# Kernel tuning notes

Measured on AMD Instinct MI355X. Metric: run time of the kernel, lower is better.

Reference implementation:

```python
import jax, jax.numpy as jnp
import numpy as np

EPSILON = 0.1
MAX_ITERATIONS = 100


def setup_inputs() -> dict:
    key = jax.random.key(0)
    k1, k2 = jax.random.split(key)
    x = jax.random.normal(k1, (16, 3, 2048), dtype=jnp.float32)
    y = jax.random.normal(k2, (16, 3, 2048), dtype=jnp.float32)
    return {"x": x, "y": y}


def reference(x, y):
    # x, y: (B, D, N) channels-first point clouds -> (B, N, D)
    xt = jnp.swapaxes(x, 1, 2)
    yt = jnp.swapaxes(y, 1, 2)
    B, N, _ = xt.shape
    # squared euclidean cost: (B, N, N)
    x2 = jnp.sum(xt * xt, axis=-1)  # (B, N)
    y2 = jnp.sum(yt * yt, axis=-1)  # (B, N)
    C = x2[:, :, None] + y2[:, None, :] - 2.0 * jnp.einsum('bnd,bmd->bnm', xt, yt)
    C = jnp.maximum(C, 0.0)  # cdist clamps negatives from cancellation
    K = jnp.exp(-C / EPSILON)

    inv_n = 1.0 / N
    u0 = jnp.full((B, N), inv_n, dtype=x.dtype)
    v0 = jnp.full((B, N), inv_n, dtype=x.dtype)

    def step(carry, _):
        u, _v = carry
        v = inv_n / (jnp.einsum('bnm,bn->bm', K, u) + 1e-8)  # K^T u
        u = inv_n / (jnp.einsum('bnm,bm->bn', K, v) + 1e-8)  # K v
        return (u, v), None

    (u, v), _ = jax.lax.scan(step, (u0, v0), None, length=MAX_ITERATIONS)
    # sum(plan * C) / B where plan = u[:,:,None] * K * v[:,None,:]
    return jnp.einsum('bn,bnm,bm->', u, K * C, v) / B
```

## Files before the change

kernel.cpp:

```cpp
#include <hip/hip_runtime.h>
#include <hip/hip_bf16.h>

#define NB 16
#define NN 2048
#define G  64
#define ITERS 100

static constexpr float INV_N = 1.0f / (float)NN;
static constexpr float NEG_INV_EPS = -10.0f;

__device__ __forceinline__ float bfl(unsigned int p) { return __uint_as_float(p << 16); }
__device__ __forceinline__ float bfh(unsigned int p) { return __uint_as_float(p & 0xffff0000u); }
__device__ __forceinline__ unsigned short f2bf(float f) {
    unsigned int u = __float_as_uint(f);
    unsigned int r = (u + 0x7fffu + ((u >> 16) & 1u)) >> 16;
    return (unsigned short)r;
}
__device__ __forceinline__ float fastrcp(float x) { return __builtin_amdgcn_rcpf(x); }

__global__ __launch_bounds__(256) void build_K(const float* __restrict__ x,
                                               const float* __restrict__ y,
                                               unsigned short* __restrict__ K) {
    const int n = blockIdx.x, b = blockIdx.y, tid = threadIdx.x;
    const float* xb = x + (size_t)b * 3 * NN;
    const float* yb = y + (size_t)b * 3 * NN;
    const float x0 = xb[n], x1 = xb[NN + n], x2 = xb[2 * NN + n];
    const float xs = x0 * x0 + x1 * x1 + x2 * x2;
    const int m0 = tid * 8;

    const float4 a0 = *(const float4*)(yb + m0);
    const float4 a1 = *(const float4*)(yb + m0 + 4);
    const float4 b0 = *(const float4*)(yb + NN + m0);
    const float4 b1 = *(const float4*)(yb + NN + m0 + 4);
    const float4 c0 = *(const float4*)(yb + 2 * NN + m0);
    const float4 c1 = *(const float4*)(yb + 2 * NN + m0 + 4);
    const float yy0[8] = {a0.x, a0.y, a0.z, a0.w, a1.x, a1.y, a1.z, a1.w};
    const float yy1[8] = {b0.x, b0.y, b0.z, b0.w, b1.x, b1.y, b1.z, b1.w};
    const float yy2[8] = {c0.x, c0.y, c0.z, c0.w, c1.x, c1.y, c1.z, c1.w};

    unsigned short kk[8];
#pragma unroll
    for (int j = 0; j < 8; ++j) {
        const float ys  = yy0[j] * yy0[j] + yy1[j] * yy1[j] + yy2[j] * yy2[j];
        const float dot = x0 * yy0[j] + x1 * yy1[j] + x2 * yy2[j];
        const float C   = fmaxf(xs + ys - 2.0f * dot, 0.0f);
        kk[j] = f2bf(__expf(NEG_INV_EPS * C));
    }
    uint4 pk;
    pk.x = (unsigned int)kk[0] | ((unsigned int)kk[1] << 16);
    pk.y = (unsigned int)kk[2] | ((unsigned int)kk[3] << 16);
    pk.z = (unsigned int)kk[4] | ((unsigned int)kk[5] << 16);
    pk.w = (unsigned int)kk[6] | ((unsigned int)kk[7] << 16);
    *(uint4*)(K + ((size_t)(b * NN + n)) * NN + m0) = pk;
}

__global__ __launch_bounds__(256) void reduce_v(const float* __restrict__ PART,
                                                float* __restrict__ VV) {
    const int t = blockIdx.x * 256 + threadIdx.x;
    const int b = t >> 11, m = t & (NN - 1);
    const float* p = PART + (size_t)(b * G) * NN + m;
    float s = 0.0f;
#pragma unroll 8
    for (int g = 0; g < G; ++g) s += p[(size_t)g * NN];
    VV[t] = INV_N * fastrcp(s + 1e-8f);
}

__global__ __launch_bounds__(256) void fused_pass(const unsigned short* __restrict__ K,
                                                  const float* __restrict__ VV,
                                                  float* __restrict__ u_out,
                                                  float* __restrict__ PART,
                                                  int first) {
    const int g = blockIdx.x, b = blockIdx.y, tid = threadIdx.x;
    const int w = tid >> 6, l = tid & 63;

    float v[4][8];
    if (!first) {
        const float* vb = VV + b * NN;
#pragma unroll
        for (int s = 0; s < 4; ++s) {
            const float4 p0 = *(const float4*)(vb + s * 512 + l * 8);
            const float4 p1 = *(const float4*)(vb + s * 512 + l * 8 + 4);
            v[s][0] = p0.x; v[s][1] = p0.y; v[s][2] = p0.z; v[s][3] = p0.w;
            v[s][4] = p1.x; v[s][5] = p1.y; v[s][6] = p1.z; v[s][7] = p1.w;
        }
    }

    float acc[4][8];
#pragma unroll
    for (int s = 0; s < 4; ++s)
#pragma unroll
        for (int j = 0; j < 8; ++j) acc[s][j] = 0.0f;

#pragma unroll 2
    for (int r = 0; r < 8; ++r) {
        const int n = g * 32 + w * 8 + r;
        const unsigned short* Kp = K + ((size_t)(b * NN + n)) * NN + l * 8;
        uint4 kv[4];
#pragma unroll
        for (int s = 0; s < 4; ++s) kv[s] = *(const uint4*)(Kp + s * 512);

        float u;
        if (first) {
            u = INV_N;
        } else {
            float a0 = 0, a1 = 0, a2 = 0, a3 = 0, a4 = 0, a5 = 0, a6 = 0, a7 = 0;
#pragma unroll
            for (int s = 0; s < 4; ++s) {
                a0 = fmaf(bfl(kv[s].x), v[s][0], a0);
                a1 = fmaf(bfh(kv[s].x), v[s][1], a1);
                a2 = fmaf(bfl(kv[s].y), v[s][2], a2);
                a3 = fmaf(bfh(kv[s].y), v[s][3], a3);
                a4 = fmaf(bfl(kv[s].z), v[s][4], a4);
                a5 = fmaf(bfh(kv[s].z), v[s][5], a5);
                a6 = fmaf(bfl(kv[s].w), v[s][6], a6);
                a7 = fmaf(bfh(kv[s].w), v[s][7], a7);
            }
            float d = ((a0 + a1) + (a2 + a3)) + ((a4 + a5) + (a6 + a7));
#pragma unroll
            for (int off = 32; off > 0; off >>= 1) d += __shfl_xor(d, off, 64);
            u = INV_N * fastrcp(d + 1e-8f);
        }
        if (l == 0) u_out[b * NN + n] = u;

#pragma unroll
        for (int s = 0; s < 4; ++s) {
            acc[s][0] = fmaf(bfl(kv[s].x), u, acc[s][0]);
            acc[s][1] = fmaf(bfh(kv[s].x), u, acc[s][1]);
            acc[s][2] = fmaf(bfl(kv[s].y), u, acc[s][2]);
            acc[s][3] = fmaf(bfh(kv[s].y), u, acc[s][3]);
            acc[s][4] = fmaf(bfl(kv[s].z), u, acc[s][4]);
            acc[s][5] = fmaf(bfh(kv[s].z), u, acc[s][5]);
            acc[s][6] = fmaf(bfl(kv[s].w), u, acc[s][6]);
            acc[s][7] = fmaf(bfh(kv[s].w), u, acc[s][7]);
        }
    }

    __shared__ float lds[4][NN];
#pragma unroll
    for (int s = 0; s < 4; ++s) {
        *(float4*)&lds[w][s * 512 + l * 8]     = make_float4(acc[s][0], acc[s][1], acc[s][2], acc[s][3]);
        *(float4*)&lds[w][s * 512 + l * 8 + 4] = make_float4(acc[s][4], acc[s][5], acc[s][6], acc[s][7]);
    }
    __syncthreads();
    float o[8];
#pragma unroll
    for (int j = 0; j < 8; ++j)
        o[j] = (lds[0][tid * 8 + j] + lds[1][tid * 8 + j]) +
               (lds[2][tid * 8 + j] + lds[3][tid * 8 + j]);
    float* p = PART + ((size_t)(b * G + g)) * NN + tid * 8;
    *(float4*)(p)     = make_float4(o[0], o[1], o[2], o[3]);
    *(float4*)(p + 4) = make_float4(o[4], o[5], o[6], o[7]);
}

__global__ __launch_bounds__(256) void final_sum(const unsigned short* __restrict__ K,
                                                 const float* __restrict__ x,
                                                 const float* __restrict__ y,
                                                 const float* __restrict__ VV,
                                                 const float* __restrict__ u_in,
                                                 float* __restrict__ out) {
    const int g = blockIdx.x, b = blockIdx.y, tid = threadIdx.x;
    const int w = tid >> 6, l = tid & 63;
    const float* vb = VV + b * NN;

    float v[4][8];
#pragma unroll
    for (int s = 0; s < 4; ++s) {
        const float4 p0 = *(const float4*)(vb + s * 512 + l * 8);
        const float4 p1 = *(const float4*)(vb + s * 512 + l * 8 + 4);
        v[s][0] = p0.x; v[s][1] = p0.y; v[s][2] = p0.z; v[s][3] = p0.w;
        v[s][4] = p1.x; v[s][5] = p1.y; v[s][6] = p1.z; v[s][7] = p1.w;
    }

    const float* xb = x + (size_t)b * 3 * NN;
    const float* yb = y + (size_t)b * 3 * NN;
    float lacc = 0.0f;

    for (int r = 0; r < 8; ++r) {
        const int n = g * 32 + w * 8 + r;
        const float x0 = xb[n], x1 = xb[NN + n], x2 = xb[2 * NN + n];
        const float xs = x0 * x0 + x1 * x1 + x2 * x2;
        const float un = u_in[b * NN + n];
        const unsigned short* Kp = K + ((size_t)(b * NN + n)) * NN + l * 8;
        float racc = 0.0f;
#pragma unroll
        for (int s = 0; s < 4; ++s) {
            const int m0 = s * 512 + l * 8;
            const uint4 kv = *(const uint4*)(Kp + s * 512);
            const float4 a0 = *(const float4*)(yb + m0);
            const float4 a1 = *(const float4*)(yb + m0 + 4);
            const float4 b0 = *(const float4*)(yb + NN + m0);
            const float4 b1 = *(const float4*)(yb + NN + m0 + 4);
            const float4 c0 = *(const float4*)(yb + 2 * NN + m0);
            const float4 c1 = *(const float4*)(yb + 2 * NN + m0 + 4);
            const float ky[8]  = {bfl(kv.x), bfh(kv.x), bfl(kv.y), bfh(kv.y),
                                  bfl(kv.z), bfh(kv.z), bfl(kv.w), bfh(kv.w)};
            const float yy0[8] = {a0.x, a0.y, a0.z, a0.w, a1.x, a1.y, a1.z, a1.w};
            const float yy1[8] = {b0.x, b0.y, b0.z, b0.w, b1.x, b1.y, b1.z, b1.w};
            const float yy2[8] = {c0.x, c0.y, c0.z, c0.w, c1.x, c1.y, c1.z, c1.w};
#pragma unroll
            for (int j = 0; j < 8; ++j) {
                const float ys  = yy0[j] * yy0[j] + yy1[j] * yy1[j] + yy2[j] * yy2[j];
                const float dot = x0 * yy0[j] + x1 * yy1[j] + x2 * yy2[j];
                const float C   = fmaxf(xs + ys - 2.0f * dot, 0.0f);
                racc = fmaf(ky[j] * C, v[s][j], racc);
            }
        }
        lacc = fmaf(un, racc, lacc);
    }
#pragma unroll
    for (int off = 32; off > 0; off >>= 1) lacc += __shfl_xor(lacc, off, 64);
    __shared__ float red[4];
    if (l == 0) red[w] = lacc;
    __syncthreads();
    if (tid == 0) atomicAdd(out, (red[0] + red[1] + red[2] + red[3]) * (1.0f / (float)NB));
}

extern "C" void kernel_launch(void* const* d_in, const int* in_sizes, int n_in,
                              void* d_out, int out_size, void* d_ws, size_t ws_size,
                              hipStream_t stream) {
    const float* x = (const float*)d_in[0];
    const float* y = (const float*)d_in[1];
    float* out = (float*)d_out;
    char* ws = (char*)d_ws;

    unsigned short* K = (unsigned short*)ws;
    const size_t KBYTES = (size_t)NB * NN * NN * 2;
    float* PART = (float*)(ws + KBYTES);
    const size_t PARTN = (size_t)NB * G * NN;
    float* VV = PART + PARTN;
    float* ub = VV + (size_t)NB * NN;

    hipMemsetAsync(out, 0, sizeof(float), stream);

    build_K<<<dim3(NN, NB), 256, 0, stream>>>(x, y, K);

    fused_pass<<<dim3(G, NB), 256, 0, stream>>>(K, VV, ub, PART, 1);
    for (int i = 0; i < ITERS; ++i) {
        reduce_v<<<dim3(NB * NN / 256), 256, 0, stream>>>(PART, VV);
        fused_pass<<<dim3(G, NB), 256, 0, stream>>>(K, VV, ub, PART, 0);
    }
    final_sum<<<dim3(G, NB), 256, 0, stream>>>(K, x, y, VV, ub, out);
}
```

Before: 3.093 ms.

## Store Sinkhorn kernel matrix in FP8 with per-row power-of-two scaling

```diff
diff --git a/kernel.cpp b/kernel.cpp
--- a/kernel.cpp
+++ b/kernel.cpp
@@ -1,27 +1,29 @@
 #include <hip/hip_runtime.h>
-#include <hip/hip_bf16.h>
 
 #define NB 16
 #define NN 2048
 #define G  64
 #define ITERS 100
 
+typedef float v2f __attribute__((ext_vector_type(2)));
+
 static constexpr float INV_N = 1.0f / (float)NN;
 static constexpr float NEG_INV_EPS = -10.0f;
 
-__device__ __forceinline__ float bfl(unsigned int p) { return __uint_as_float(p << 16); }
-__device__ __forceinline__ float bfh(unsigned int p) { return __uint_as_float(p & 0xffff0000u); }
-__device__ __forceinline__ unsigned short f2bf(float f) {
-    unsigned int u = __float_as_uint(f);
-    unsigned int r = (u + 0x7fffu + ((u >> 16) & 1u)) >> 16;
-    return (unsigned short)r;
-}
 __device__ __forceinline__ float fastrcp(float x) { return __builtin_amdgcn_rcpf(x); }
+
+__device__ __forceinline__ void dec4(unsigned int u, float& f0, float& f1, float& f2, float& f3) {
+    v2f lo = __builtin_amdgcn_cvt_pk_f32_fp8((int)u, false);
+    v2f hi = __builtin_amdgcn_cvt_pk_f32_fp8((int)u, true);
+    f0 = lo[0]; f1 = lo[1]; f2 = hi[0]; f3 = hi[1];
+}
 
 __global__ __launch_bounds__(256) void build_K(const float* __restrict__ x,
                                                const float* __restrict__ y,
-                                               unsigned short* __restrict__ K) {
+                                               unsigned char* __restrict__ K8,
+                                               float* __restrict__ INVS) {
     const int n = blockIdx.x, b = blockIdx.y, tid = threadIdx.x;
+    const int w = tid >> 6, l = tid & 63;
     const float* xb = x + (size_t)b * 3 * NN;
     const float* yb = y + (size_t)b * 3 * NN;
     const float x0 = xb[n], x1 = xb[NN + n], x2 = xb[2 * NN + n];
@@ -38,20 +40,34 @@
     const float yy1[8] = {b0.x, b0.y, b0.z, b0.w, b1.x, b1.y, b1.z, b1.w};
     const float yy2[8] = {c0.x, c0.y, c0.z, c0.w, c1.x, c1.y, c1.z, c1.w};
 
-    unsigned short kk[8];
+    float k[8];
 #pragma unroll
     for (int j = 0; j < 8; ++j) {
         const float ys  = yy0[j] * yy0[j] + yy1[j] * yy1[j] + yy2[j] * yy2[j];
         const float dot = x0 * yy0[j] + x1 * yy1[j] + x2 * yy2[j];
         const float C   = fmaxf(xs + ys - 2.0f * dot, 0.0f);
-        kk[j] = f2bf(__expf(NEG_INV_EPS * C));
-    }
-    uint4 pk;
-    pk.x = (unsigned int)kk[0] | ((unsigned int)kk[1] << 16);
-    pk.y = (unsigned int)kk[2] | ((unsigned int)kk[3] << 16);
-    pk.z = (unsigned int)kk[4] | ((unsigned int)kk[5] << 16);
-    pk.w = (unsigned int)kk[6] | ((unsigned int)kk[7] << 16);
-    *(uint4*)(K + ((size_t)(b * NN + n)) * NN + m0) = pk;
+        k[j] = __expf(NEG_INV_EPS * C);
+    }
+
+    float mx = fmaxf(fmaxf(fmaxf(k[0], k[1]), fmaxf(k[2], k[3])),
+                     fmaxf(fmaxf(k[4], k[5]), fmaxf(k[6], k[7])));
+#pragma unroll
+    for (int off = 32; off > 0; off >>= 1) mx = fmaxf(mx, __shfl_xor(mx, off, 64));
+    __shared__ float red[4];
+    if (l == 0) red[w] = mx;
+    __syncthreads();
+    mx = fmaxf(fmaxf(red[0], red[1]), fmaxf(red[2], red[3]));
+    mx = fmaxf(mx, 1e-30f);
+    const int e = (int)((__float_as_uint(mx) >> 23) & 0xffu) - 127;
+    const float sc = __uint_as_float((unsigned)(127 - e) << 23);
+    if (tid == 0) INVS[b * NN + n] = __uint_as_float((unsigned)(127 + e) << 23);
+
+    int p0 = __builtin_amdgcn_cvt_pk_fp8_f32(k[0] * sc, k[1] * sc, 0, false);
+    p0     = __builtin_amdgcn_cvt_pk_fp8_f32(k[2] * sc, k[3] * sc, p0, true);
+    int p1 = __builtin_amdgcn_cvt_pk_fp8_f32(k[4] * sc, k[5] * sc, 0, false);
+    p1     = __builtin_amdgcn_cvt_pk_fp8_f32(k[6] * sc, k[7] * sc, p1, true);
+    uint2 pk; pk.x = (unsigned)p0; pk.y = (unsigned)p1;
+    *(uint2*)(K8 + ((size_t)(b * NN + n)) * NN + m0) = pk;
 }
 
 __global__ __launch_bounds__(256) void reduce_v(const float* __restrict__ PART,
@@ -65,81 +81,83 @@
     VV[t] = INV_N * fastrcp(s + 1e-8f);
 }
 
-__global__ __launch_bounds__(256) void fused_pass(const unsigned short* __restrict__ K,
-                                                  const float* __restrict__ VV,
-                                                  float* __restrict__ u_out,
-                                                  float* __restrict__ PART,
-                                                  int first) {
+#define DOT4(wrd, s, j0) { float f0_, f1_, f2_, f3_; dec4(wrd, f0_, f1_, f2_, f3_);          \
+    d0 = fmaf(f0_, v[s][j0+0], d0); d1 = fmaf(f1_, v[s][j0+1], d1);                          \
+    d2 = fmaf(f2_, v[s][j0+2], d2); d3 = fmaf(f3_, v[s][j0+3], d3); }
+#define ACC4(wrd, s, j0) { float f0_, f1_, f2_, f3_; dec4(wrd, f0_, f1_, f2_, f3_);          \
+    acc[s][j0+0] = fmaf(f0_, uw, acc[s][j0+0]); acc[s][j0+1] = fmaf(f1_, uw, acc[s][j0+1]);  \
+    acc[s][j0+2] = fmaf(f2_, uw, acc[s][j0+2]); acc[s][j0+3] = fmaf(f3_, uw, acc[s][j0+3]); }
+
+__global__ __launch_bounds__(256, 4) void fused_pass(const unsigned char* __restrict__ K8,
+                                                     const float* __restrict__ VV,
+                                                     const float* __restrict__ INVS,
+                                                     float* __restrict__ u_out,
+                                                     float* __restrict__ PART,
+                                                     int first) {
     const int g = blockIdx.x, b = blockIdx.y, tid = threadIdx.x;
     const int w = tid >> 6, l = tid & 63;
 
-    float v[4][8];
+    float v[2][16];
     if (!first) {
         const float* vb = VV + b * NN;
 #pragma unroll
-        for (int s = 0; s < 4; ++s) {
-            const float4 p0 = *(const float4*)(vb + s * 512 + l * 8);
-            const float4 p1 = *(const float4*)(vb + s * 512 + l * 8 + 4);
-            v[s][0] = p0.x; v[s][1] = p0.y; v[s][2] = p0.z; v[s][3] = p0.w;
-            v[s][4] = p1.x; v[s][5] = p1.y; v[s][6] = p1.z; v[s][7] = p1.w;
+        for (int s = 0; s < 2; ++s) {
+            const float4 q0 = *(const float4*)(vb + s * 1024 + l * 16);
+            const float4 q1 = *(const float4*)(vb + s * 1024 + l * 16 + 4);
+            const float4 q2 = *(const float4*)(vb + s * 1024 + l * 16 + 8);
+            const float4 q3 = *(const float4*)(vb + s * 1024 + l * 16 + 12);
+            v[s][0]  = q0.x; v[s][1]  = q0.y; v[s][2]  = q0.z; v[s][3]  = q0.w;
+            v[s][4]  = q1.x; v[s][5]  = q1.y; v[s][6]  = q1.z; v[s][7]  = q1.w;
+            v[s][8]  = q2.x; v[s][9]  = q2.y; v[s][10] = q2.z; v[s][11] = q2.w;
+            v[s][12] = q3.x; v[s][13] = q3.y; v[s][14] = q3.z; v[s][15] = q3.w;
         }
-    }
-
-    float acc[4][8];
-#pragma unroll
-    for (int s = 0; s < 4; ++s)
-#pragma unroll
-        for (int j = 0; j < 8; ++j) acc[s][j] = 0.0f;
+    } else {
+#pragma unroll
+        for (int s = 0; s < 2; ++s)
+#pragma unroll
+            for (int j = 0; j < 16; ++j) v[s][j] = 0.0f;
+    }
+
+    float acc[2][16];
+#pragma unroll
+    for (int s = 0; s < 2; ++s)
+#pragma unroll
+        for (int j = 0; j < 16; ++j) acc[s][j] = 0.0f;
+
+    const int row0 = g * 32 + w * 8;
+    const unsigned char* Kb = K8 + ((size_t)(b * NN + row0)) * NN + l * 16;
+    const float* invp = INVS + b * NN + row0;
 
 #pragma unroll 2
     for (int r = 0; r < 8; ++r) {
-        const int n = g * 32 + w * 8 + r;
-        const unsigned short* Kp = K + ((size_t)(b * NN + n)) * NN + l * 8;
-        uint4 kv[4];
-#pragma unroll
-        for (int s = 0; s < 4; ++s) kv[s] = *(const uint4*)(Kp + s * 512);
-
+        const uint4 kv0 = *(const uint4*)(Kb + (size_t)r * NN);
+        const uint4 kv1 = *(const uint4*)(Kb + (size_t)r * NN + 1024);
+        const float invs = invp[r];
         float u;
         if (first) {
             u = INV_N;
         } else {
-            float a0 = 0, a1 = 0, a2 = 0, a3 = 0, a4 = 0, a5 = 0, a6 = 0, a7 = 0;
-#pragma unroll
-            for (int s = 0; s < 4; ++s) {
-                a0 = fmaf(bfl(kv[s].x), v[s][0], a0);
-                a1 = fmaf(bfh(kv[s].x), v[s][1], a1);
-                a2 = fmaf(bfl(kv[s].y), v[s][2], a2);
-                a3 = fmaf(bfh(kv[s].y), v[s][3], a3);
-                a4 = fmaf(bfl(kv[s].z), v[s][4], a4);
-                a5 = fmaf(bfh(kv[s].z), v[s][5], a5);
-                a6 = fmaf(bfl(kv[s].w), v[s][6], a6);
-                a7 = fmaf(bfh(kv[s].w), v[s][7], a7);
-            }
-            float d = ((a0 + a1) + (a2 + a3)) + ((a4 + a5) + (a6 + a7));
+            float d0 = 0, d1 = 0, d2 = 0, d3 = 0;
+            DOT4(kv0.x, 0, 0);  DOT4(kv0.y, 0, 4);  DOT4(kv0.z, 0, 8);  DOT4(kv0.w, 0, 12);
+            DOT4(kv1.x, 1, 0);  DOT4(kv1.y, 1, 4);  DOT4(kv1.z, 1, 8);  DOT4(kv1.w, 1, 12);
+            float d = (d0 + d1) + (d2 + d3);
 #pragma unroll
             for (int off = 32; off > 0; off >>= 1) d += __shfl_xor(d, off, 64);
-            u = INV_N * fastrcp(d + 1e-8f);
+            u = INV_N * fastrcp(d * invs + 1e-8f);
         }
-        if (l == 0) u_out[b * NN + n] = u;
-
-#pragma unroll
-        for (int s = 0; s < 4; ++s) {
-            acc[s][0] = fmaf(bfl(kv[s].x), u, acc[s][0]);
-            acc[s][1] = fmaf(bfh(kv[s].x), u, acc[s][1]);
-            acc[s][2] = fmaf(bfl(kv[s].y), u, acc[s][2]);
-            acc[s][3] = fmaf(bfh(kv[s].y), u, acc[s][3]);
-            acc[s][4] = fmaf(bfl(kv[s].z), u, acc[s][4]);
-            acc[s][5] = fmaf(bfh(kv[s].z), u, acc[s][5]);
-            acc[s][6] = fmaf(bfl(kv[s].w), u, acc[s][6]);
-            acc[s][7] = fmaf(bfh(kv[s].w), u, acc[s][7]);
-        }
+        if (l == 0) u_out[b * NN + row0 + r] = u;
+        const float uw = u * invs;
+        ACC4(kv0.x, 0, 0);  ACC4(kv0.y, 0, 4);  ACC4(kv0.z, 0, 8);  ACC4(kv0.w, 0, 12);
+        ACC4(kv1.x, 1, 0);  ACC4(kv1.y, 1, 4);  ACC4(kv1.z, 1, 8);  ACC4(kv1.w, 1, 12);
     }
 
     __shared__ float lds[4][NN];
 #pragma unroll
-    for (int s = 0; s < 4; ++s) {
-        *(float4*)&lds[w][s * 512 + l * 8]     = make_float4(acc[s][0], acc[s][1], acc[s][2], acc[s][3]);
-        *(float4*)&lds[w][s * 512 + l * 8 + 4] = make_float4(acc[s][4], acc[s][5], acc[s][6], acc[s][7]);
+    for (int s = 0; s < 2; ++s) {
+        *(float4*)&lds[w][s * 1024 + l * 16]      = make_float4(acc[s][0],  acc[s][1],  acc[s][2],  acc[s][3]);
+        *(float4*)&lds[w][s * 1024 + l * 16 + 4]  = make_float4(acc[s][4],  acc[s][5],  acc[s][6],  acc[s][7]);
+        *(float4*)&lds[w][s * 1024 + l * 16 + 8]  = make_float4(acc[s][8],  acc[s][9],  acc[s][10], acc[s][11]);
+        *(float4*)&lds[w][s * 1024 + l * 16 + 12] = make_float4(acc[s][12], acc[s][13], acc[s][14], acc[s][15]);
     }
     __syncthreads();
     float o[8];
@@ -152,10 +170,11 @@
     *(float4*)(p + 4) = make_float4(o[4], o[5], o[6], o[7]);
 }
 
-__global__ __launch_bounds__(256) void final_sum(const unsigned short* __restrict__ K,
+__global__ __launch_bounds__(256) void final_sum(const unsigned char* __restrict__ K8,
                                                  const float* __restrict__ x,
                                                  const float* __restrict__ y,
                                                  const float* __restrict__ VV,
+                                                 const float* __restrict__ INVS,
                                                  const float* __restrict__ u_in,
                                                  float* __restrict__ out) {
     const int g = blockIdx.x, b = blockIdx.y, tid = threadIdx.x;
@@ -180,20 +199,22 @@
         const float x0 = xb[n], x1 = xb[NN + n], x2 = xb[2 * NN + n];
         const float xs = x0 * x0 + x1 * x1 + x2 * x2;
         const float un = u_in[b * NN + n];
-        const unsigned short* Kp = K + ((size_t)(b * NN + n)) * NN + l * 8;
+        const float invs = INVS[b * NN + n];
+        const unsigned char* Kp = K8 + ((size_t)(b * NN + n)) * NN + l * 8;
         float racc = 0.0f;
 #pragma unroll
         for (int s = 0; s < 4; ++s) {
             const int m0 = s * 512 + l * 8;
-            const uint4 kv = *(const uint4*)(Kp + s * 512);
+            const uint2 kv = *(const uint2*)(Kp + s * 512);
+            float ky[8];
+            dec4(kv.x, ky[0], ky[1], ky[2], ky[3]);
+            dec4(kv.y, ky[4], ky[5], ky[6], ky[7]);
             const float4 a0 = *(const float4*)(yb + m0);
             const float4 a1 = *(const float4*)(yb + m0 + 4);
             const float4 b0 = *(const float4*)(yb + NN + m0);
             const float4 b1 = *(const float4*)(yb + NN + m0 + 4);
             const float4 c0 = *(const float4*)(yb + 2 * NN + m0);
             const float4 c1 = *(const float4*)(yb + 2 * NN + m0 + 4);
-            const float ky[8]  = {bfl(kv.x), bfh(kv.x), bfl(kv.y), bfh(kv.y),
-                                  bfl(kv.z), bfh(kv.z), bfl(kv.w), bfh(kv.w)};
             const float yy0[8] = {a0.x, a0.y, a0.z, a0.w, a1.x, a1.y, a1.z, a1.w};
             const float yy1[8] = {b0.x, b0.y, b0.z, b0.w, b1.x, b1.y, b1.z, b1.w};
             const float yy2[8] = {c0.x, c0.y, c0.z, c0.w, c1.x, c1.y, c1.z, c1.w};
@@ -205,7 +226,7 @@
                 racc = fmaf(ky[j] * C, v[s][j], racc);
             }
         }
-        lacc = fmaf(un, racc, lacc);
+        lacc = fmaf(un * invs, racc, lacc);
     }
 #pragma unroll
     for (int off = 32; off > 0; off >>= 1) lacc += __shfl_xor(lacc, off, 64);
@@ -223,21 +244,22 @@
     float* out = (float*)d_out;
     char* ws = (char*)d_ws;
 
-    unsigned short* K = (unsigned short*)ws;
-    const size_t KBYTES = (size_t)NB * NN * NN * 2;
+    unsigned char* K8 = (unsigned char*)ws;
+    const size_t KBYTES = (size_t)NB * NN * NN;
     float* PART = (float*)(ws + KBYTES);
     const size_t PARTN = (size_t)NB * G * NN;
-    float* VV = PART + PARTN;
-    float* ub = VV + (size_t)NB * NN;
+    float* VV   = PART + PARTN;
+    float* ub   = VV + (size_t)NB * NN;
+    float* INVS = ub + (size_t)NB * NN;
 
     hipMemsetAsync(out, 0, sizeof(float), stream);
 
-    build_K<<<dim3(NN, NB), 256, 0, stream>>>(x, y, K);
-
-    fused_pass<<<dim3(G, NB), 256, 0, stream>>>(K, VV, ub, PART, 1);
+    build_K<<<dim3(NN, NB), 256, 0, stream>>>(x, y, K8, INVS);
+
+    fused_pass<<<dim3(G, NB), 256, 0, stream>>>(K8, VV, INVS, ub, PART, 1);
     for (int i = 0; i < ITERS; ++i) {
         reduce_v<<<dim3(NB * NN / 256), 256, 0, stream>>>(PART, VV);
-        fused_pass<<<dim3(G, NB), 256, 0, stream>>>(K, VV, ub, PART, 0);
-    }
-    final_sum<<<dim3(G, NB), 256, 0, stream>>>(K, x, y, VV, ub, out);
-}
+        fused_pass<<<dim3(G, NB), 256, 0, stream>>>(K8, VV, INVS, ub, PART, 0);
+    }
+    final_sum<<<dim3(G, NB), 256, 0, stream>>>(K8, x, y, VV, INVS, ub, out);
+}
```

After: 6.412 ms. 107% more time.
